# Performance work log

Hardware: AMD Instinct MI355X
Metric: run time of the kernel (lower is better)

Reference implementation:

```python
import jax, jax.numpy as jnp
import numpy as np

N = 4096          # num_nodes
E = 65536         # num edges (avg degree 16)
WALK_LENGTH = 16
OUT_DIM = 8


def setup_inputs() -> dict:
    key = jax.random.key(0)
    k1, k2 = jax.random.split(key, 2)
    edge_index = jax.random.randint(k1, (2, E), 0, N, dtype=jnp.int64)
    # nn.Linear(walk_length, out_dim): weight [out_dim, walk_length], bias [out_dim]
    linear_w = (jax.random.normal(k2, (OUT_DIM, WALK_LENGTH), jnp.float32)
                / np.float32(np.sqrt(WALK_LENGTH)))
    linear_b = jnp.zeros((OUT_DIM,), jnp.float32)
    return {"edge_index": edge_index, "num_nodes": N,
            "linear_w": linear_w, "linear_b": linear_b}


def reference(edge_index, num_nodes, linear_w, linear_b):
    row, col = edge_index[0], edge_index[1]
    # out-degree via scatter_add, clamped to >= 1
    deg = jnp.zeros((num_nodes,), jnp.float32).at[row].add(1.0)
    deg = jnp.maximum(deg, 1.0)
    rw_values = 1.0 / deg[row]                              # [E]
    # random-walk transition matrix P[row, col] = 1/deg[row]
    # (.at[].add sums duplicate edges, matching coalesce())
    P = jnp.zeros((num_nodes, num_nodes), jnp.float32).at[row, col].add(rw_values)
    Pt = P.T

    def step(cur, _):
        cur = Pt @ cur                                      # [N, N]
        return cur, jnp.diagonal(cur)                       # k-step return probs

    cur0 = jnp.eye(num_nodes, dtype=jnp.float32)
    _, diags = jax.lax.scan(step, cur0, None, length=WALK_LENGTH)
    rw_diag = diags.T                                       # [N, walk_length]
    return rw_diag @ linear_w.T + linear_b                  # [N, out_dim]
```

## Files before the change

kernel.cpp:

```cpp
#include <hip/hip_runtime.h>
#include <hip/hip_fp16.h>
#include <hip/hip_fp8.h>

#define NNODES 4096
#define LWALK 16
#define ODIM 8

#define FP8_SCALE 256.0f
#define FP8_INV   0.00390625f
#define FP8_INV2  1.52587890625e-05f

typedef unsigned int uint4n __attribute__((ext_vector_type(4)));
typedef float float2n __attribute__((ext_vector_type(2)));

__device__ __forceinline__ void dec8f(unsigned int lo, unsigned int hi, float* f) {
#if __has_builtin(__builtin_amdgcn_cvt_pk_f32_fp8)
    float2n p;
    p = __builtin_amdgcn_cvt_pk_f32_fp8((int)lo, false); f[0] = p.x; f[1] = p.y;
    p = __builtin_amdgcn_cvt_pk_f32_fp8((int)lo, true);  f[2] = p.x; f[3] = p.y;
    p = __builtin_amdgcn_cvt_pk_f32_fp8((int)hi, false); f[4] = p.x; f[5] = p.y;
    p = __builtin_amdgcn_cvt_pk_f32_fp8((int)hi, true);  f[6] = p.x; f[7] = p.y;
#else
    unsigned int w[2] = {lo, hi};
    const unsigned char* b = (const unsigned char*)w;
#pragma unroll
    for (int i = 0; i < 8; ++i) {
        __hip_fp8_e4m3 t; t.__x = b[i]; f[i] = (float)t;
    }
#endif
}

__device__ __forceinline__ void enc8f(const float* a, unsigned int* lo,
                                      unsigned int* hi) {
#if __has_builtin(__builtin_amdgcn_cvt_pk_fp8_f32)
    int l = 0, h = 0;
    l = __builtin_amdgcn_cvt_pk_fp8_f32(a[0], a[1], l, false);
    l = __builtin_amdgcn_cvt_pk_fp8_f32(a[2], a[3], l, true);
    h = __builtin_amdgcn_cvt_pk_fp8_f32(a[4], a[5], h, false);
    h = __builtin_amdgcn_cvt_pk_fp8_f32(a[6], a[7], h, true);
    *lo = (unsigned int)l; *hi = (unsigned int)h;
#else
    unsigned char b[8];
#pragma unroll
    for (int i = 0; i < 8; ++i)
        b[i] = __hip_cvt_float_to_fp8(a[i], __HIP_SATFINITE, __HIP_E4M3);
    unsigned int w[2];
    __builtin_memcpy(w, b, 8);
    *lo = w[0]; *hi = w[1];
#endif
}

__device__ __forceinline__ void dec16f(uint4n w, float* f) {
    dec8f(w.x, w.y, f);
    dec8f(w.z, w.w, f + 8);
}

__device__ __forceinline__ uint4n enc16f(const float* a) {
    uint4n o;
    unsigned int lo, hi;
    enc8f(a, &lo, &hi);     o.x = lo; o.y = hi;
    enc8f(a + 8, &lo, &hi); o.z = lo; o.w = hi;
    return o;
}

__global__ void detect_fmt_k(const void* ei, int E, int* flag) {
    if (blockIdx.x == 0 && threadIdx.x == 0) {
        const long long* p = (const long long*)ei;
        int ok = 1;
        for (int i = 0; i < 64; ++i) {
            long long v = p[i];
            if (v < 0 || v >= NNODES) { ok = 0; break; }
        }
        *flag = ok;
    }
}

__device__ __forceinline__ int load_idx(const void* p, int i, int fmt) {
    if (fmt) return (int)((const long long*)p)[i];
    return ((const int*)p)[i];
}

__global__ void build_deg_cnt_k(const void* ei, int E, int* deg, int* cnt,
                                const int* fmt) {
    int e = blockIdx.x * blockDim.x + threadIdx.x;
    if (e >= E) return;
    int f = *fmt;
    int r = load_idx(ei, e, f);
    int c = load_idx(ei, E + e, f);
    atomicAdd(&deg[r], 1);
    atomicAdd(&cnt[c], 1);
}

__global__ void scan_k(const int* __restrict__ cnt, int* __restrict__ rowptr,
                       int* __restrict__ cursor) {
    __shared__ int sm[1024];
    int tid = threadIdx.x;
    int v0 = (cnt[4 * tid + 0] + 3) & ~3;
    int v1 = (cnt[4 * tid + 1] + 3) & ~3;
    int v2 = (cnt[4 * tid + 2] + 3) & ~3;
    int v3 = (cnt[4 * tid + 3] + 3) & ~3;
    int tsum = v0 + v1 + v2 + v3;
    sm[tid] = tsum;
    __syncthreads();
    int val = tsum;
    for (int off = 1; off < 1024; off <<= 1) {
        int t = (tid >= off) ? sm[tid - off] : 0;
        __syncthreads();
        val += t;
        sm[tid] = val;
        __syncthreads();
    }
    int excl = val - tsum;
    int p0 = excl, p1 = excl + v0, p2 = p1 + v1, p3 = p2 + v2;
    rowptr[4 * tid + 0] = p0; rowptr[4 * tid + 1] = p1;
    rowptr[4 * tid + 2] = p2; rowptr[4 * tid + 3] = p3;
    cursor[4 * tid + 0] = p0; cursor[4 * tid + 1] = p1;
    cursor[4 * tid + 2] = p2; cursor[4 * tid + 3] = p3;
    if (tid == 1023) rowptr[4096] = val;
}

__global__ void fill_pad_k(const void* ei, int E, const int* __restrict__ deg,
                           int* cursor, const int* __restrict__ rowptr,
                           uint2* __restrict__ epad, const int* fmt) {
    int e = blockIdx.x * blockDim.x + threadIdx.x;
    if (e < E) {
        int f = *fmt;
        int r = load_idx(ei, e, f);
        int c = load_idx(ei, E + e, f);
        int pos = atomicAdd(&cursor[c], 1);
        int d = deg[r];
        float v = 1.0f / (float)(d < 1 ? 1 : d);
        epad[pos] = make_uint2((unsigned)r, __float_as_uint(v));
    }
}

__global__ void pad_fill_k(const int* __restrict__ rowptr,
                           const int* __restrict__ cursor,
                           uint2* __restrict__ epad) {
    int c = blockIdx.x * blockDim.x + threadIdx.x;
    if (c >= NNODES) return;
    for (int p = cursor[c]; p < rowptr[c + 1]; ++p)
        epad[p] = make_uint2(0u, 0u);
}

__global__ __launch_bounds__(256) void x2build_k(
    const int* __restrict__ rowptr, const uint2* __restrict__ epad,
    unsigned char* __restrict__ Y8, float* __restrict__ rw) {
    __shared__ float row[NNODES];
    __shared__ float dia1;
    const int c = blockIdx.x;
    const int t = threadIdx.x;
    for (int i = t; i < NNODES; i += 256) row[i] = 0.f;
    if (t == 0) dia1 = 0.f;
    __syncthreads();
    const int beg = rowptr[c], end = rowptr[c + 1];
    const int g = t >> 4;
    const int l = t & 15;
    for (int i1 = beg + g; i1 < end; i1 += 16) {
        uint2 e1 = epad[i1];
        float v = __uint_as_float(e1.y);
        if (v != 0.f) {
            int r = (int)e1.x;
            if (r == c && l == 0) atomicAdd(&dia1, v);
            int b2 = rowptr[r], n2 = rowptr[r + 1];
            for (int j = b2 + l; j < n2; j += 16) {
                uint2 e2 = epad[j];
                float w = __uint_as_float(e2.y);
                if (w != 0.f) atomicAdd(&row[e2.x], v * w);
            }
        }
    }
    __syncthreads();
    if (t == 0) {
        rw[c * LWALK + 0] = dia1;
        rw[c * LWALK + 1] = row[c];
    }
    float f[16];
    const int base = t * 16;
#pragma unroll
    for (int u = 0; u < 16; ++u) f[u] = row[base + u] * FP8_SCALE;
    uint4n o = enc16f(f);
    __builtin_nontemporal_store(o, (uint4n*)(Y8 + (size_t)c * NNODES + base));
}

__global__ __launch_bounds__(256) void fused8_k(
    const unsigned char* __restrict__ X8, unsigned char* __restrict__ Y8,
    const int* __restrict__ rowptr, const uint2* __restrict__ epad,
    float* __restrict__ rw, int kcol,
    const unsigned char* __restrict__ PA, const unsigned char* __restrict__ PB,
    int colO, int colE, int nspmm) {
    __shared__ __half bt[64][66];
    __shared__ __half ct[64][66];
    const int bid = blockIdx.x;
    if (bid < nspmm) {
        const int slab = bid & 7;
        const int lane = threadIdx.x & 63;
        const int half = lane >> 5;
        const int li = lane & 31;
        const int c =
            __builtin_amdgcn_readfirstlane((bid >> 3) * 4 + (threadIdx.x >> 6));
        const int colo = slab * 512 + li * 16;
        const unsigned char* Xs = X8 + colo;
        const int beg = rowptr[c], end = rowptr[c + 1];
        float a[16];
#pragma unroll
        for (int u = 0; u < 16; ++u) a[u] = 0.f;
        for (int e = beg; e < end; e += 4) {
            uint2 e0 = epad[e + half];
            uint2 e1 = epad[e + 2 + half];
            uint4n x0 = *(const uint4n*)(Xs + (size_t)e0.x * NNODES);
            uint4n x1 = *(const uint4n*)(Xs + (size_t)e1.x * NNODES);
            float f[16];
            float v;
            v = __uint_as_float(e0.y);
            dec16f(x0, f);
#pragma unroll
            for (int u = 0; u < 16; ++u) a[u] = fmaf(f[u], v, a[u]);
            v = __uint_as_float(e1.y);
            dec16f(x1, f);
#pragma unroll
            for (int u = 0; u < 16; ++u) a[u] = fmaf(f[u], v, a[u]);
        }
#pragma unroll
        for (int u = 0; u < 16; ++u) a[u] += __shfl_xor(a[u], 32);
        if (half == 0) {
            if ((c >> 9) == slab && li == ((c & 511) >> 4)) {
                float d = 0.f;
#pragma unroll
                for (int u = 0; u < 16; ++u)
                    if ((c & 15) == u) d = a[u];
                rw[c * LWALK + kcol] = d * FP8_INV;
            }
            uint4n o = enc16f(a);
            __builtin_nontemporal_store(
                o, (uint4n*)(Y8 + (size_t)c * NNODES + colo));
        }
    } else {
        const int pb = bid - nspmm;
        const int i0 = (pb & 63) * 64;
        const int Jbeg = (pb >> 6) * (NNODES / 16);
        const int Jend = Jbeg + (NNODES / 16);
        const int t = threadIdx.x;
        const int li = t >> 2;
        const int q = t & 3;
        const int c0 = q * 16;
        float accO = 0.f, accE = 0.f;
        for (int J = Jbeg; J < Jend; J += 64) {
            uint4n b16 = __builtin_nontemporal_load(
                (const uint4n*)(PB + (size_t)(J + li) * NNODES + i0 + c0));
            uint4n g16 = __builtin_nontemporal_load(
                (const uint4n*)(PA + (size_t)(J + li) * NNODES + i0 + c0));
            __syncthreads();
            float bf[16], gf[16];
            dec16f(b16, bf);
            dec16f(g16, gf);
#pragma unroll
            for (int s = 0; s < 16; ++s) {
                bt[c0 + s][li] = __float2half(bf[s]);
                ct[c0 + s][li] = __float2half(gf[s]);
            }
            __syncthreads();
            uint4n a16 = __builtin_nontemporal_load(
                (const uint4n*)(PA + (size_t)(i0 + li) * NNODES + J + c0));
            float af[16];
            dec16f(a16, af);
#pragma unroll
            for (int s = 0; s < 16; ++s) {
                accO = fmaf(af[s], __half2float(bt[li][c0 + s]), accO);
                accE = fmaf(af[s], __half2float(ct[li][c0 + s]), accE);
            }
        }
        accO += __shfl_xor(accO, 1);
        accO += __shfl_xor(accO, 2);
        accE += __shfl_xor(accE, 1);
        accE += __shfl_xor(accE, 2);
        if (q == 0) {
            atomicAdd(&rw[(i0 + li) * LWALK + colO], accO * FP8_INV2);
            atomicAdd(&rw[(i0 + li) * LWALK + colE], accE * FP8_INV2);
        }
    }
}

__global__ __launch_bounds__(256) void finale_k(
    const unsigned char* __restrict__ PA, const unsigned char* __restrict__ PB,
    float* __restrict__ rw, const float* __restrict__ W,
    const float* __restrict__ b, float* __restrict__ out, int npair) {
    __shared__ __half bt[64][66];
    __shared__ __half ct[64][66];
    const int bid = blockIdx.x;
    if (bid < npair) {
        const int pb = bid;
        const int i0 = (pb & 63) * 64;
        const int Jbeg = (pb >> 6) * (NNODES / 16);
        const int Jend = Jbeg + (NNODES / 16);
        const int t = threadIdx.x;
        const int li = t >> 2;
        const int q = t & 3;
        const int c0 = q * 16;
        float accO = 0.f, accE = 0.f;
        for (int J = Jbeg; J < Jend; J += 64) {
            uint4n b16 = __builtin_nontemporal_load(
                (const uint4n*)(PB + (size_t)(J + li) * NNODES + i0 + c0));
            uint4n g16 = __builtin_nontemporal_load(
                (const uint4n*)(PA + (size_t)(J + li) * NNODES + i0 + c0));
            __syncthreads();
            float bf[16], gf[16];
            dec16f(b16, bf);
            dec16f(g16, gf);
#pragma unroll
            for (int s = 0; s < 16; ++s) {
                bt[c0 + s][li] = __float2half(bf[s]);
                ct[c0 + s][li] = __float2half(gf[s]);
            }
            __syncthreads();
            uint4n a16 = __builtin_nontemporal_load(
                (const uint4n*)(PA + (size_t)(i0 + li) * NNODES + J + c0));
            float af[16];
            dec16f(a16, af);
#pragma unroll
            for (int s = 0; s < 16; ++s) {
                accO = fmaf(af[s], __half2float(bt[li][c0 + s]), accO);
                accE = fmaf(af[s], __half2float(ct[li][c0 + s]), accE);
            }
        }
        accO += __shfl_xor(accO, 1);
        accO += __shfl_xor(accO, 2);
        accE += __shfl_xor(accE, 1);
        accE += __shfl_xor(accE, 2);
        if (q == 0) {
            atomicAdd(&rw[(i0 + li) * LWALK + 14], accO * FP8_INV2);
            atomicAdd(&rw[(i0 + li) * LWALK + 15], accE * FP8_INV2);
        }
    }
}

__global__ void linear_k(const float* __restrict__ rw, const float* __restrict__ W,
                         const float* __restrict__ b, float* __restrict__ out) {
    int i = blockIdx.x * blockDim.x + threadIdx.x;
    if (i >= NNODES * ODIM) return;
    int s = i >> 3, d = i & 7;
    float acc = b[d];
#pragma unroll
    for (int k = 0; k < LWALK; ++k)
        acc = fmaf(rw[s * LWALK + k], W[d * LWALK + k], acc);
    out[i] = acc;
}

extern "C" void kernel_launch(void* const* d_in, const int* in_sizes, int n_in,
                              void* d_out, int out_size, void* d_ws, size_t ws_size,
                              hipStream_t stream) {
    const void* ei = d_in[0];
    int E = in_sizes[0] / 2;
    const float* W = (const float*)d_in[2];
    const float* bias = (const float*)d_in[3];
    float* out = (float*)d_out;

    char* ws = (char*)d_ws;
    size_t off = 0;
    auto alloc = [&](size_t bytes) -> char* {
        char* p = ws + off;
        off = (off + bytes + 255) & ~(size_t)255;
        return p;
    };
    int* flag = (int*)alloc(4);
    int* deg = (int*)alloc(NNODES * 4);
    int* cnt = (int*)alloc(NNODES * 4);
    int* rowptr = (int*)alloc((NNODES + 1) * 4);
    int* cursor = (int*)alloc(NNODES * 4);
    uint2* epad = (uint2*)alloc(((size_t)E + 4 * NNODES) * 8);
    float* rw = (float*)alloc(NNODES * LWALK * 4);
    unsigned char* A = (unsigned char*)alloc((size_t)NNODES * NNODES);
    unsigned char* B = (unsigned char*)alloc((size_t)NNODES * NNODES);
    unsigned char* C = (unsigned char*)alloc((size_t)NNODES * NNODES);

    (void)hipMemsetAsync(deg, 0, NNODES * 4, stream);
    (void)hipMemsetAsync(cnt, 0, NNODES * 4, stream);
    (void)hipMemsetAsync(rw, 0, NNODES * LWALK * 4, stream);
    detect_fmt_k<<<1, 64, 0, stream>>>(ei, E, flag);
    build_deg_cnt_k<<<(E + 255) / 256, 256, 0, stream>>>(ei, E, deg, cnt, flag);
    scan_k<<<1, 1024, 0, stream>>>(cnt, rowptr, cursor);
    fill_pad_k<<<(E + 255) / 256, 256, 0, stream>>>(ei, E, deg, cursor, rowptr,
                                                    epad, flag);
    pad_fill_k<<<(NNODES + 255) / 256, 256, 0, stream>>>(rowptr, cursor, epad);

    x2build_k<<<NNODES, 256, 0, stream>>>(rowptr, epad, A, rw);

    const int SG = 8192;
    fused8_k<<<SG, 256, 0, stream>>>(A, B, rowptr, epad, rw, 2, nullptr, nullptr, 0, 0, SG);
    fused8_k<<<SG, 256, 0, stream>>>(B, C, rowptr, epad, rw, 3, nullptr, nullptr, 0, 0, SG);
    fused8_k<<<SG, 256, 0, stream>>>(C, A, rowptr, epad, rw, 4, nullptr, nullptr, 0, 0, SG);
    fused8_k<<<SG + 1024, 256, 0, stream>>>(A, B, rowptr, epad, rw, 5, A, C, 8, 9, SG);
    fused8_k<<<SG + 1024, 256, 0, stream>>>(B, C, rowptr, epad, rw, 6, B, A, 10, 11, SG);
    fused8_k<<<SG + 1024, 256, 0, stream>>>(C, A, rowptr, epad, rw, 7, C, B, 12, 13, SG);
    finale_k<<<1024, 256, 0, stream>>>(A, C, rw, W, bias, out, 1024);
    linear_k<<<(NNODES * ODIM + 255) / 256, 256, 0, stream>>>(rw, W, bias, out);
}
```

Before: 328.8 us.

## Use persistent grid with per-block SpMM loop followed by split-K pair products

Replaces the 8192-block SpMM grid and the separate 1024 pair-product blocks with a 2048-block grid. Each block loops over four row groups for the sparse product, then, when enabled, runs a pair-product tile whose J range is halved so that 2048 blocks cover the work. The goal is fewer blocks, less launch and tail imbalance, and every block doing both kinds of work instead of the heterogeneous blocks competing. The cost is that the pair work now runs serially after each block's SpMM loop rather than alongside it, and the extra split adds twice as many atomics into rw.

Measured after the change: 331.7 us. About the same (+0.9%).

```diff
diff --git a/kernel.cpp b/kernel.cpp
--- a/kernel.cpp
+++ b/kernel.cpp
@@ -188,19 +188,20 @@
     const int* __restrict__ rowptr, const uint2* __restrict__ epad,
     float* __restrict__ rw, int kcol,
     const unsigned char* __restrict__ PA, const unsigned char* __restrict__ PB,
-    int colO, int colE, int nspmm) {
+    int colO, int colE, int dopair) {
     __shared__ __half bt[64][66];
     __shared__ __half ct[64][66];
     const int bid = blockIdx.x;
-    if (bid < nspmm) {
-        const int slab = bid & 7;
-        const int lane = threadIdx.x & 63;
-        const int half = lane >> 5;
-        const int li = lane & 31;
-        const int c =
-            __builtin_amdgcn_readfirstlane((bid >> 3) * 4 + (threadIdx.x >> 6));
-        const int colo = slab * 512 + li * 16;
-        const unsigned char* Xs = X8 + colo;
+    const int slab = bid & 7;
+    const int worker = bid >> 3;
+    const int lane = threadIdx.x & 63;
+    const int half = lane >> 5;
+    const int li = lane & 31;
+    const int wv = threadIdx.x >> 6;
+    const int colo = slab * 512 + li * 16;
+    const unsigned char* Xs = X8 + colo;
+    for (int cg = worker; cg < 1024; cg += 256) {
+        const int c = __builtin_amdgcn_readfirstlane(cg * 4 + wv);
         const int beg = rowptr[c], end = rowptr[c + 1];
         float a[16];
 #pragma unroll
@@ -235,39 +236,42 @@
             __builtin_nontemporal_store(
                 o, (uint4n*)(Y8 + (size_t)c * NNODES + colo));
         }
-    } else {
-        const int pb = bid - nspmm;
+    }
+    if (dopair) {
+        const int pb = bid >> 1;
+        const int jh = bid & 1;
         const int i0 = (pb & 63) * 64;
-        const int Jbeg = (pb >> 6) * (NNODES / 16);
-        const int Jend = Jbeg + (NNODES / 16);
+        const int Jbeg = (pb >> 6) * (NNODES / 16) + jh * (NNODES / 32);
+        const int Jend = Jbeg + (NNODES / 32);
         const int t = threadIdx.x;
-        const int li = t >> 2;
+        const int pli = t >> 2;
         const int q = t & 3;
         const int c0 = q * 16;
         float accO = 0.f, accE = 0.f;
+        __syncthreads();
         for (int J = Jbeg; J < Jend; J += 64) {
             uint4n b16 = __builtin_nontemporal_load(
-                (const uint4n*)(PB + (size_t)(J + li) * NNODES + i0 + c0));
+                (const uint4n*)(PB + (size_t)(J + pli) * NNODES + i0 + c0));
             uint4n g16 = __builtin_nontemporal_load(
-                (const uint4n*)(PA + (size_t)(J + li) * NNODES + i0 + c0));
+                (const uint4n*)(PA + (size_t)(J + pli) * NNODES + i0 + c0));
             __syncthreads();
             float bf[16], gf[16];
             dec16f(b16, bf);
             dec16f(g16, gf);
 #pragma unroll
             for (int s = 0; s < 16; ++s) {
-                bt[c0 + s][li] = __float2half(bf[s]);
-                ct[c0 + s][li] = __float2half(gf[s]);
+                bt[c0 + s][pli] = __float2half(bf[s]);
+                ct[c0 + s][pli] = __float2half(gf[s]);
             }
             __syncthreads();
             uint4n a16 = __builtin_nontemporal_load(
-                (const uint4n*)(PA + (size_t)(i0 + li) * NNODES + J + c0));
+                (const uint4n*)(PA + (size_t)(i0 + pli) * NNODES + J + c0));
             float af[16];
             dec16f(a16, af);
 #pragma unroll
             for (int s = 0; s < 16; ++s) {
-                accO = fmaf(af[s], __half2float(bt[li][c0 + s]), accO);
-                accE = fmaf(af[s], __half2float(ct[li][c0 + s]), accE);
+                accO = fmaf(af[s], __half2float(bt[pli][c0 + s]), accO);
+                accE = fmaf(af[s], __half2float(ct[pli][c0 + s]), accE);
             }
         }
         accO += __shfl_xor(accO, 1);
@@ -275,8 +279,8 @@
         accE += __shfl_xor(accE, 1);
         accE += __shfl_xor(accE, 2);
         if (q == 0) {
-            atomicAdd(&rw[(i0 + li) * LWALK + colO], accO * FP8_INV2);
-            atomicAdd(&rw[(i0 + li) * LWALK + colE], accE * FP8_INV2);
+            atomicAdd(&rw[(i0 + pli) * LWALK + colO], accO * FP8_INV2);
+            atomicAdd(&rw[(i0 + pli) * LWALK + colE], accE * FP8_INV2);
         }
     }
 }
@@ -289,10 +293,11 @@
     __shared__ __half ct[64][66];
     const int bid = blockIdx.x;
     if (bid < npair) {
-        const int pb = bid;
+        const int pb = bid >> 1;
+        const int jh = bid & 1;
         const int i0 = (pb & 63) * 64;
-        const int Jbeg = (pb >> 6) * (NNODES / 16);
-        const int Jend = Jbeg + (NNODES / 16);
+        const int Jbeg = (pb >> 6) * (NNODES / 16) + jh * (NNODES / 32);
+        const int Jend = Jbeg + (NNODES / 32);
         const int t = threadIdx.x;
         const int li = t >> 2;
         const int q = t & 3;
@@ -385,13 +390,13 @@
 
     x2build_k<<<NNODES, 256, 0, stream>>>(rowptr, epad, A, rw);
 
-    const int SG = 8192;
-    fused8_k<<<SG, 256, 0, stream>>>(A, B, rowptr, epad, rw, 2, nullptr, nullptr, 0, 0, SG);
-    fused8_k<<<SG, 256, 0, stream>>>(B, C, rowptr, epad, rw, 3, nullptr, nullptr, 0, 0, SG);
-    fused8_k<<<SG, 256, 0, stream>>>(C, A, rowptr, epad, rw, 4, nullptr, nullptr, 0, 0, SG);
-    fused8_k<<<SG + 1024, 256, 0, stream>>>(A, B, rowptr, epad, rw, 5, A, C, 8, 9, SG);
-    fused8_k<<<SG + 1024, 256, 0, stream>>>(B, C, rowptr, epad, rw, 6, B, A, 10, 11, SG);
-    fused8_k<<<SG + 1024, 256, 0, stream>>>(C, A, rowptr, epad, rw, 7, C, B, 12, 13, SG);
-    finale_k<<<1024, 256, 0, stream>>>(A, C, rw, W, bias, out, 1024);
+    const int PG = 2048;
+    fused8_k<<<PG, 256, 0, stream>>>(A, B, rowptr, epad, rw, 2, nullptr, nullptr, 0, 0, 0);
+    fused8_k<<<PG, 256, 0, stream>>>(B, C, rowptr, epad, rw, 3, nullptr, nullptr, 0, 0, 0);
+    fused8_k<<<PG, 256, 0, stream>>>(C, A, rowptr, epad, rw, 4, nullptr, nullptr, 0, 0, 0);
+    fused8_k<<<PG, 256, 0, stream>>>(A, B, rowptr, epad, rw, 5, A, C, 8, 9, 1);
+    fused8_k<<<PG, 256, 0, stream>>>(B, C, rowptr, epad, rw, 6, B, A, 10, 11, 1);
+    fused8_k<<<PG, 256, 0, stream>>>(C, A, rowptr, epad, rw, 7, C, B, 12, 13, 1);
+    finale_k<<<PG, 256, 0, stream>>>(A, C, rw, W, bias, out, PG);
     linear_k<<<(NNODES * ODIM + 255) / 256, 256, 0, stream>>>(rw, W, bias, out);
 }
```
